# Optimization experiments

Hardware: AMD Instinct MI355X
Metric: run time of the kernel (lower is better)

Reference implementation:

```python
import jax, jax.numpy as jnp
import numpy as np

EMBED = 768
HEADS = 12
HEAD_DIM = EMBED // HEADS  # 64
SCALE = float(EMBED) ** 0.5  # NOTE: module scales by sqrt(embed_size), not sqrt(head_dim)


def setup_inputs() -> dict:
    key = jax.random.key(0)
    k_x, k_wqkv, k_bqkv, k_wp, k_bp = jax.random.split(key, 5)
    x = jax.random.normal(k_x, (16, 1024, EMBED), dtype=jnp.float32)
    # nn.Linear(embed, 3*embed): weight [out,in], bias [out]
    w_qkv = jax.random.normal(k_wqkv, (3 * EMBED, EMBED), dtype=jnp.float32) * 0.02
    b_qkv = jax.random.normal(k_bqkv, (3 * EMBED,), dtype=jnp.float32) * 0.02
    w_proj = jax.random.normal(k_wp, (EMBED, EMBED), dtype=jnp.float32) * 0.02
    b_proj = jax.random.normal(k_bp, (EMBED,), dtype=jnp.float32) * 0.02
    return {"x": x, "w_qkv": w_qkv, "b_qkv": b_qkv, "w_proj": w_proj, "b_proj": b_proj}


def reference(x, w_qkv, b_qkv, w_proj, b_proj):
    B, N, C = x.shape
    qkv = x @ w_qkv.T + b_qkv                       # [B, N, 3C]
    # rearrange 'b n (h d qkv) -> qkv b h n d': qkv index is INNERMOST factor
    qkv = qkv.reshape(B, N, HEADS, HEAD_DIM, 3)
    q = jnp.transpose(qkv[..., 0], (0, 2, 1, 3))    # [B, H, N, D]
    k = jnp.transpose(qkv[..., 1], (0, 2, 1, 3))
    v = jnp.transpose(qkv[..., 2], (0, 2, 1, 3))
    attn = jnp.einsum('bhqd,bhkd->bhqk', q, k) / SCALE
    attn = jax.nn.softmax(attn, axis=-1)
    out = jnp.einsum('bhqk,bhkd->bhqd', attn, v)    # [B, H, N, D]
    out = jnp.transpose(out, (0, 2, 1, 3)).reshape(B, N, C)
    return out @ w_proj.T + b_proj
```

## Files before the change

### kernel.cpp

```cpp
#include <hip/hip_runtime.h>

typedef short bf16x8 __attribute__((ext_vector_type(8)));
typedef float f32x4 __attribute__((ext_vector_type(4)));
typedef float f32x16 __attribute__((ext_vector_type(16)));

#define Q_PRESCALE 0.05205877485199535f

__device__ __forceinline__ unsigned short f2bf(float f) {
  unsigned u = __float_as_uint(f);
  u += 0x7fffu + ((u >> 16) & 1u);
  return (unsigned short)(u >> 16);
}

__device__ __forceinline__ int cvt_pk_bf16(float lo, float hi) {
  int r;
  asm("v_cvt_pk_bf16_f32 %0, %1, %2" : "=v"(r) : "v"(lo), "v"(hi));
  return r;
}

__device__ __forceinline__ float fast_exp2(float x) {
  return __builtin_amdgcn_exp2f(x);
}

__device__ __forceinline__ float cross_half_add(float x) {
  float y;
  asm("v_mov_b32 %0, %1" : "=v"(y) : "v"(x));
  asm("v_permlane32_swap_b32 %0, %1" : "+v"(x), "+v"(y));
  return x + y;
}

__device__ __forceinline__ void gload_lds16(const void* g, void* l) {
  __builtin_amdgcn_global_load_lds(
      (const __attribute__((address_space(1))) void*)g,
      (__attribute__((address_space(3))) void*)l, 16, 0, 0);
}

__global__ __launch_bounds__(256) void prep_kernel(
    const float* __restrict__ x, unsigned short* __restrict__ xb,
    const float* __restrict__ w_qkv, unsigned short* __restrict__ wqkvb,
    const float* __restrict__ w_proj, unsigned short* __restrict__ wprojb) {
  const int bid = blockIdx.x;
  if (bid < 12288) {
    int i = bid * 256 + threadIdx.x;
    float4 v = ((const float4*)x)[i];
    int2 o;
    o.x = cvt_pk_bf16(v.x, v.y);
    o.y = cvt_pk_bf16(v.z, v.w);
    *(int2*)((ushort4*)xb + i) = o;
  } else if (bid < 14016) {
    int i = (bid - 12288) * 256 + threadIdx.x;
    int col = i / 192, i4 = i % 192;
    int c = col / 768, rem = col % 768;
    int h = rem >> 6, d = rem & 63;
    int orig = h * 192 + d * 3 + c;
    float4 v = ((const float4*)(w_qkv + (size_t)orig * 768))[i4];
    int2 o;
    o.x = cvt_pk_bf16(v.x, v.y);
    o.y = cvt_pk_bf16(v.z, v.w);
    *(int2*)((ushort4*)(wqkvb + (size_t)col * 768) + i4) = o;
  } else {
    int i = (bid - 14016) * 256 + threadIdx.x;
    float4 v = ((const float4*)w_proj)[i];
    int2 o;
    o.x = cvt_pk_bf16(v.x, v.y);
    o.y = cvt_pk_bf16(v.z, v.w);
    *(int2*)((ushort4*)wprojb + i) = o;
  }
}

template<int EPI, int NT, int NBUF>
__global__ __launch_bounds__(256) void gemm_bt(
    const unsigned short* __restrict__ A,
    const unsigned short* __restrict__ B,
    const float* __restrict__ bias,
    void* __restrict__ out0,
    unsigned short* __restrict__ Kb,
    unsigned short* __restrict__ VTb) {
  constexpr int K = 768;
  __shared__ __align__(16) unsigned short smem[NBUF * 8192];

  const int tid = threadIdx.x;
  const int w = tid >> 6, lane = tid & 63;
  const int g = lane >> 4, qq = lane & 15;
  const int wr = w >> 1, wc = w & 1;

  const int nwg = gridDim.x, chunk = nwg >> 3;
  const int id = blockIdx.x;
  const int id2 = (id & 7) * chunk + (id >> 3);
  const int bx = id2 % NT, by = id2 / NT;
  const int rowb = by * 128;

  const unsigned short* Ab = A + (size_t)rowb * K;
  const unsigned short* Bb = B + (size_t)bx * 128 * K;

  f32x4 acc[4][4];
#pragma unroll
  for (int i = 0; i < 4; i++)
#pragma unroll
    for (int j = 0; j < 4; j++) acc[i][j] = (f32x4){0.f, 0.f, 0.f, 0.f};

  const int j0 = tid, j1 = tid + 256;
  const int l0 = j0 >> 3, s0 = (j0 & 7) ^ (l0 & 7);
  const int l1 = j1 >> 3, s1 = (j1 & 7) ^ (l1 & 7);
  const size_t off0 = (size_t)(2 * l0 + (s0 >> 2)) * K + (s0 & 3) * 8;
  const size_t off1 = (size_t)(2 * l1 + (s1 >> 2)) * K + (s1 & 3) * 8;

  int aoff[4], boff[4];
#pragma unroll
  for (int mi = 0; mi < 4; mi++) {
    int row = wr * 64 + mi * 16 + qq;
    aoff[mi] = (row >> 1) * 128 + (((g + (row & 1) * 4) ^ ((row >> 1) & 7)) * 16);
    row = wc * 64 + mi * 16 + qq;
    boff[mi] = (row >> 1) * 128 + (((g + (row & 1) * 4) ^ ((row >> 1) & 7)) * 16);
  }

  auto stageg = [&](int sb, int k0) {
    unsigned short* base = &smem[sb * 8192];
    gload_lds16(Ab + off0 + k0, base + j0 * 8);
    gload_lds16(Ab + off1 + k0, base + j1 * 8);
    gload_lds16(Bb + off0 + k0, base + 4096 + j0 * 8);
    gload_lds16(Bb + off1 + k0, base + 4096 + j1 * 8);
  };

#pragma unroll
  for (int p = 0; p < NBUF - 1; ++p) stageg(p, p * 32);

  for (int tg = 0; tg < 24; tg += NBUF) {
#pragma unroll
    for (int j = 0; j < NBUF; ++j) {
      const int t = tg + j;
      if constexpr (NBUF == 3) {
        if (t < 23) asm volatile("s_waitcnt vmcnt(4)" ::: "memory");
        else        asm volatile("s_waitcnt vmcnt(0)" ::: "memory");
      } else {
        if (t < 22)       asm volatile("s_waitcnt vmcnt(8)" ::: "memory");
        else if (t == 22) asm volatile("s_waitcnt vmcnt(4)" ::: "memory");
        else              asm volatile("s_waitcnt vmcnt(0)" ::: "memory");
      }
      asm volatile("s_barrier" ::: "memory");
      if (t <= 24 - NBUF) stageg((j + NBUF - 1) % NBUF, (t + NBUF - 1) * 32);

      const char* Ap = (const char*)&smem[j * 8192];
      const char* Bp = Ap + 8192;
      bf16x8 af[4], bfr[4];
#pragma unroll
      for (int mi = 0; mi < 4; mi++) af[mi] = *(const bf16x8*)(Ap + aoff[mi]);
#pragma unroll
      for (int ni = 0; ni < 4; ni++) bfr[ni] = *(const bf16x8*)(Bp + boff[ni]);
      __builtin_amdgcn_s_setprio(1);
#pragma unroll
      for (int mi = 0; mi < 4; mi++)
#pragma unroll
        for (int ni = 0; ni < 4; ni++)
          acc[mi][ni] = __builtin_amdgcn_mfma_f32_16x16x32_bf16(af[mi], bfr[ni], acc[mi][ni], 0, 0, 0);
      __builtin_amdgcn_s_setprio(0);
    }
  }

  if (EPI == 0) {
    const int c = bx / 6;
    const int h0 = (bx % 6) * 2;
    const int b = rowb >> 10, n0 = rowb & 1023;
    if (c < 2) {
      unsigned short* dst = (c == 0) ? (unsigned short*)out0 : Kb;
      const float scale = (c == 0) ? Q_PRESCALE : 1.0f;
      const int h = h0 + wc;
      const size_t bh = (size_t)(b * 12 + h);
#pragma unroll
      for (int ni = 0; ni < 4; ni++) {
        const int d = ni * 16 + qq;
        const float bv = bias[h * 192 + d * 3 + c];
#pragma unroll
        for (int mi = 0; mi < 4; mi++) {
          const int nb = n0 + wr * 64 + mi * 16 + g * 4;
          unsigned short* base = dst + (bh * 1024 + nb) * 64 + d;
          const int p0 = cvt_pk_bf16((acc[mi][ni][0] + bv) * scale,
                                     (acc[mi][ni][1] + bv) * scale);
          const int p1 = cvt_pk_bf16((acc[mi][ni][2] + bv) * scale,
                                     (acc[mi][ni][3] + bv) * scale);
          base[0]   = (unsigned short)p0;
          base[64]  = (unsigned short)((unsigned)p0 >> 16);
          base[128] = (unsigned short)p1;
          base[192] = (unsigned short)((unsigned)p1 >> 16);
        }
      }
    } else {
      unsigned short* vt = smem;
#pragma unroll
      for (int p = 0; p < 2; ++p) {
        __syncthreads();
        if (wc == p) {
#pragma unroll
          for (int ni = 0; ni < 4; ni++) {
            const int d = ni * 16 + qq;
            const float bv = bias[(h0 + p) * 192 + d * 3 + 2];
#pragma unroll
            for (int mi = 0; mi < 4; mi++) {
              int2 pk;
              pk.x = cvt_pk_bf16(acc[mi][ni][0] + bv, acc[mi][ni][1] + bv);
              pk.y = cvt_pk_bf16(acc[mi][ni][2] + bv, acc[mi][ni][3] + bv);
              *(int2*)&vt[d * 136 + wr * 64 + mi * 16 + g * 4] = pk;
            }
          }
        }
        __syncthreads();
        const size_t bhp = (size_t)(b * 12 + h0 + p);
        const int dd = tid >> 2;
#pragma unroll
        for (int j = 0; j < 4; ++j) {
          const int ch = (tid & 3) + j * 4;
          uint4 vv = *(const uint4*)&vt[dd * 136 + ch * 8];
          const int n = n0 + ch * 8;
          const int tile = n >> 6;
          const int ksd = (n >> 4) & 3;
          const int tk = n & 15;
          *(uint4*)&VTb[bhp * 65536 + (size_t)tile * 4096 + ksd * 1024 + dd * 16 + tk] = vv;
        }
      }
    }
  } else {
    float* O = (float*)out0;
    const int colb = bx * 128 + wc * 64;
#pragma unroll
    for (int ni = 0; ni < 4; ni++) {
      const int col = colb + ni * 16 + qq;
      const float bv = bias[col];
#pragma unroll
      for (int mi = 0; mi < 4; mi++)
#pragma unroll
        for (int r = 0; r < 4; r++) {
          const int row = rowb + wr * 64 + mi * 16 + g * 4 + r;
          O[(size_t)row * 768 + col] = acc[mi][ni][r] + bv;
        }
    }
  }
}

__global__ __launch_bounds__(256, 3) void attn_kernel(
    const unsigned short* __restrict__ Qb,
    const unsigned short* __restrict__ Kb,
    const unsigned short* __restrict__ VTb,
    unsigned short* __restrict__ AO) {
  __shared__ unsigned short Klds[4][4096];
  const int tid = threadIdx.x;
  const int w = tid >> 6, lane = tid & 63;
  const int ql = lane & 31, hi = lane >> 5;

  const int bid = blockIdx.x;
  const int xcd = bid & 7, jj = bid >> 3;
  const int bh = xcd * 24 + (jj >> 3);
  const int qb = jj & 7;
  const int b = bh / 12, h = bh % 12;
  const int q0w = qb * 128 + w * 32;

  const unsigned short* Qh = Qb + (size_t)bh * 65536;
  const unsigned short* Kh = Kb + (size_t)bh * 65536;
  const unsigned short* Vh = VTb + (size_t)bh * 65536;

  bf16x8 qf[4];
#pragma unroll
  for (int ks = 0; ks < 4; ++ks)
    qf[ks] = *(const bf16x8*)&Qh[(size_t)(q0w + ql) * 64 + ks * 16 + hi * 8];

  float l_run = 0.f;
  f32x16 o[2];
#pragma unroll
  for (int dt = 0; dt < 2; ++dt)
#pragma unroll
    for (int i = 0; i < 16; ++i) o[dt][i] = 0.f;

  const int j0 = w * 64 + lane;
  const int r0 = j0 >> 3, s0 = j0 & 7;
  const int g0 = s0 ^ (r0 & 7) ^ ((r0 >> 2) & 6);
  const int sx = (ql & 7) ^ ((ql >> 2) & 6);

  int koff[2][4];
#pragma unroll
  for (int tt = 0; tt < 2; ++tt)
#pragma unroll
    for (int ks = 0; ks < 4; ++ks)
      koff[tt][ks] = (tt * 32 + ql) * 128 + (((ks * 2 + hi) ^ sx) * 16);
  int voff[2][4];
#pragma unroll
  for (int dt = 0; dt < 2; ++dt)
#pragma unroll
    for (int ks = 0; ks < 4; ++ks)
      voff[dt][ks] = ks * 1024 + (dt * 32 + ql) * 16 + hi * 8;

  auto stage = [&](int sb, int t0) {
    gload_lds16(Kh + (size_t)(t0 + r0) * 64 + g0 * 8, &Klds[sb][j0 * 8]);
    gload_lds16(Kh + (size_t)(t0 + r0 + 32) * 64 + g0 * 8, &Klds[sb][j0 * 8 + 2048]);
  };

  stage(0, 0);
  stage(1, 64);
  stage(2, 128);

  for (int t = 0; t < 16; ++t) {
    if (t < 14)      asm volatile("s_waitcnt vmcnt(4)" ::: "memory");
    else if (t == 14) asm volatile("s_waitcnt vmcnt(2)" ::: "memory");
    else              asm volatile("s_waitcnt vmcnt(0)" ::: "memory");
    asm volatile("s_barrier" ::: "memory");
    if (t < 13) stage((t + 3) & 3, (t + 3) * 64);

    const char* Kbuf = (const char*)&Klds[t & 3][0];
    const unsigned short* Vt = Vh + t * 4096;

    bf16x8 vf[2][4];
#pragma unroll
    for (int dt = 0; dt < 2; ++dt)
#pragma unroll
      for (int ks = 0; ks < 4; ++ks)
        vf[dt][ks] = *(const bf16x8*)&Vt[voff[dt][ks]];

    f32x16 s[2];
    __builtin_amdgcn_s_setprio(1);
#pragma unroll
    for (int tt = 0; tt < 2; ++tt) {
#pragma unroll
      for (int i = 0; i < 16; ++i) s[tt][i] = 0.f;
#pragma unroll
      for (int ks = 0; ks < 4; ++ks) {
        bf16x8 ka = *(const bf16x8*)(Kbuf + koff[tt][ks]);
        s[tt] = __builtin_amdgcn_mfma_f32_32x32x16_bf16(ka, qf[ks], s[tt], 0, 0, 0);
      }
    }
    __builtin_amdgcn_s_setprio(0);

#pragma unroll
    for (int tt = 0; tt < 2; ++tt)
#pragma unroll
      for (int i = 0; i < 16; ++i) s[tt][i] = fast_exp2(s[tt][i]);

    float r16[16];
#pragma unroll
    for (int i = 0; i < 16; ++i) r16[i] = s[0][i] + s[1][i];
    float r8[8];
#pragma unroll
    for (int i = 0; i < 8; ++i) r8[i] = r16[i] + r16[i + 8];
    float r4[4];
#pragma unroll
    for (int i = 0; i < 4; ++i) r4[i] = r8[i] + r8[i + 4];
    float rs = (r4[0] + r4[1]) + (r4[2] + r4[3]);
    l_run += cross_half_add(rs);

    union PU { int i[4]; bf16x8 h; };
    PU pb[4];
#pragma unroll
    for (int g16 = 0; g16 < 4; ++g16) {
      const int tt = g16 >> 1, rb = (g16 & 1) * 8;
      int A0, A1, B0, B1;
      float a0 = s[tt][rb + 0], a1 = s[tt][rb + 1], a2 = s[tt][rb + 2], a3 = s[tt][rb + 3];
      float b0 = s[tt][rb + 4], b1 = s[tt][rb + 5], b2 = s[tt][rb + 6], b3 = s[tt][rb + 7];
      asm("v_cvt_pk_bf16_f32 %0, %1, %2" : "=v"(A0) : "v"(a0), "v"(a1));
      asm("v_cvt_pk_bf16_f32 %0, %1, %2" : "=v"(A1) : "v"(a2), "v"(a3));
      asm("v_cvt_pk_bf16_f32 %0, %1, %2" : "=v"(B0) : "v"(b0), "v"(b1));
      asm("v_cvt_pk_bf16_f32 %0, %1, %2" : "=v"(B1) : "v"(b2), "v"(b3));
      asm("v_permlane32_swap_b32 %0, %1" : "+v"(A0), "+v"(B0));
      asm("v_permlane32_swap_b32 %0, %1" : "+v"(A1), "+v"(B1));
      pb[g16].i[0] = A0; pb[g16].i[1] = A1; pb[g16].i[2] = B0; pb[g16].i[3] = B1;
    }

    __builtin_amdgcn_s_setprio(1);
#pragma unroll
    for (int dt = 0; dt < 2; ++dt)
#pragma unroll
      for (int ks = 0; ks < 4; ++ks)
        o[dt] = __builtin_amdgcn_mfma_f32_32x32x16_bf16(vf[dt][ks], pb[ks].h, o[dt], 0, 0, 0);
    __builtin_amdgcn_s_setprio(0);
  }

  const float inv_l = 1.0f / l_run;
  unsigned short* aorow = AO + (size_t)(b * 1024 + q0w + ql) * 768 + h * 64 + hi * 4;
#pragma unroll
  for (int dt = 0; dt < 2; ++dt)
#pragma unroll
    for (int p = 0; p < 4; ++p) {
      int2 vv;
      vv.x = cvt_pk_bf16(o[dt][4 * p + 0] * inv_l, o[dt][4 * p + 1] * inv_l);
      vv.y = cvt_pk_bf16(o[dt][4 * p + 2] * inv_l, o[dt][4 * p + 3] * inv_l);
      *(int2*)&aorow[dt * 32 + 8 * p] = vv;
    }
}

extern "C" void kernel_launch(void* const* d_in, const int* in_sizes, int n_in,
                              void* d_out, int out_size, void* d_ws, size_t ws_size,
                              hipStream_t stream) {
  const float* x      = (const float*)d_in[0];
  const float* w_qkv  = (const float*)d_in[1];
  const float* b_qkv  = (const float*)d_in[2];
  const float* w_proj = (const float*)d_in[3];
  const float* b_proj = (const float*)d_in[4];

  char* ws = (char*)d_ws;
  unsigned short* xb     = (unsigned short*)(ws);
  unsigned short* Qb     = (unsigned short*)(ws + 25165824);
  unsigned short* Kb     = (unsigned short*)(ws + 50331648);
  unsigned short* VTb    = (unsigned short*)(ws + 75497472);
  unsigned short* wqkvb  = (unsigned short*)(ws + 100663296);
  unsigned short* wprojb = (unsigned short*)(ws + 104202240);
  unsigned short* AO = xb;

  prep_kernel<<<14592, 256, 0, stream>>>(x, xb, w_qkv, wqkvb, w_proj, wprojb);

  gemm_bt<0, 18, 4><<<2304, 256, 0, stream>>>(xb, wqkvb, b_qkv, (void*)Qb, Kb, VTb);
  attn_kernel<<<1536, 256, 0, stream>>>(Qb, Kb, VTb, AO);
  gemm_bt<1, 6, 4><<<768, 256, 0, stream>>>(AO, wprojb, b_proj, d_out, nullptr, nullptr);
}
```

Before: 188.3 us.

## Switch K staging to double-buffered 128-key tiles with one barrier per tile

Restructures the attention kernel's K pipeline from a 4-deep ring of 64-key tiles to a 2-deep ring of 128-key tiles. Each iteration now waits for all loads, issues the next tile's prefetch, and processes two 64-key halves, so it runs 8 barriers instead of 16. LDS use stays the same, but prefetch depth drops to one tile and the full vmcnt(0) wait may expose load latency. The V register loads inside each half could also lose overlap with the K prefetch.

```diff
diff --git a/kernel.cpp b/kernel.cpp
--- a/kernel.cpp
+++ b/kernel.cpp
@@ -241,7 +241,7 @@
     const unsigned short* __restrict__ Kb,
     const unsigned short* __restrict__ VTb,
     unsigned short* __restrict__ AO) {
-  __shared__ unsigned short Klds[4][4096];
+  __shared__ unsigned short Klds[2][8192];
   const int tid = threadIdx.x;
   const int w = tid >> 6, lane = tid & 63;
   const int ql = lane & 31, hi = lane >> 5;
@@ -269,9 +269,14 @@
 #pragma unroll
     for (int i = 0; i < 16; ++i) o[dt][i] = 0.f;
 
-  const int j0 = w * 64 + lane;
-  const int r0 = j0 >> 3, s0 = j0 & 7;
-  const int g0 = s0 ^ (r0 & 7) ^ ((r0 >> 2) & 6);
+  int kgofs[4];
+#pragma unroll
+  for (int k = 0; k < 4; ++k) {
+    const int j = tid + k * 256;
+    const int r = j >> 3, s = j & 7;
+    const int g0 = s ^ (r & 7) ^ ((r >> 2) & 6);
+    kgofs[k] = r * 64 + g0 * 8;
+  }
   const int sx = (ql & 7) ^ ((ql >> 2) & 6);
 
   int koff[2][4];
@@ -287,87 +292,90 @@
     for (int ks = 0; ks < 4; ++ks)
       voff[dt][ks] = ks * 1024 + (dt * 32 + ql) * 16 + hi * 8;
 
-  auto stage = [&](int sb, int t0) {
-    gload_lds16(Kh + (size_t)(t0 + r0) * 64 + g0 * 8, &Klds[sb][j0 * 8]);
-    gload_lds16(Kh + (size_t)(t0 + r0 + 32) * 64 + g0 * 8, &Klds[sb][j0 * 8 + 2048]);
+  auto stage = [&](int sb, int t) {
+    const unsigned short* Kt = Kh + (size_t)t * 8192;
+#pragma unroll
+    for (int k = 0; k < 4; ++k)
+      gload_lds16(Kt + kgofs[k], &Klds[sb][(tid + k * 256) * 8]);
   };
 
   stage(0, 0);
-  stage(1, 64);
-  stage(2, 128);
-
-  for (int t = 0; t < 16; ++t) {
-    if (t < 14)      asm volatile("s_waitcnt vmcnt(4)" ::: "memory");
-    else if (t == 14) asm volatile("s_waitcnt vmcnt(2)" ::: "memory");
-    else              asm volatile("s_waitcnt vmcnt(0)" ::: "memory");
+
+  for (int t = 0; t < 8; ++t) {
+    asm volatile("s_waitcnt vmcnt(0)" ::: "memory");
     asm volatile("s_barrier" ::: "memory");
-    if (t < 13) stage((t + 3) & 3, (t + 3) * 64);
-
-    const char* Kbuf = (const char*)&Klds[t & 3][0];
-    const unsigned short* Vt = Vh + t * 4096;
-
-    bf16x8 vf[2][4];
-#pragma unroll
-    for (int dt = 0; dt < 2; ++dt)
-#pragma unroll
-      for (int ks = 0; ks < 4; ++ks)
-        vf[dt][ks] = *(const bf16x8*)&Vt[voff[dt][ks]];
-
-    f32x16 s[2];
-    __builtin_amdgcn_s_setprio(1);
-#pragma unroll
-    for (int tt = 0; tt < 2; ++tt) {
-#pragma unroll
-      for (int i = 0; i < 16; ++i) s[tt][i] = 0.f;
-#pragma unroll
-      for (int ks = 0; ks < 4; ++ks) {
-        bf16x8 ka = *(const bf16x8*)(Kbuf + koff[tt][ks]);
-        s[tt] = __builtin_amdgcn_mfma_f32_32x32x16_bf16(ka, qf[ks], s[tt], 0, 0, 0);
+    if (t < 7) stage((t + 1) & 1, t + 1);
+
+    const char* Kbuf = (const char*)&Klds[t & 1][0];
+
+#pragma unroll
+    for (int half = 0; half < 2; ++half) {
+      const int kb = half * 8192;
+      const unsigned short* Vt = Vh + (size_t)t * 8192 + half * 4096;
+
+      bf16x8 vf[2][4];
+#pragma unroll
+      for (int dt = 0; dt < 2; ++dt)
+#pragma unroll
+        for (int ks = 0; ks < 4; ++ks)
+          vf[dt][ks] = *(const bf16x8*)&Vt[voff[dt][ks]];
+
+      f32x16 s[2];
+      __builtin_amdgcn_s_setprio(1);
+#pragma unroll
+      for (int tt = 0; tt < 2; ++tt) {
+#pragma unroll
+        for (int i = 0; i < 16; ++i) s[tt][i] = 0.f;
+#pragma unroll
+        for (int ks = 0; ks < 4; ++ks) {
+          bf16x8 ka = *(const bf16x8*)(Kbuf + kb + koff[tt][ks]);
+          s[tt] = __builtin_amdgcn_mfma_f32_32x32x16_bf16(ka, qf[ks], s[tt], 0, 0, 0);
+        }
       }
+      __builtin_amdgcn_s_setprio(0);
+
+#pragma unroll
+      for (int tt = 0; tt < 2; ++tt)
+#pragma unroll
+        for (int i = 0; i < 16; ++i) s[tt][i] = fast_exp2(s[tt][i]);
+
+      float r16[16];
+#pragma unroll
+      for (int i = 0; i < 16; ++i) r16[i] = s[0][i] + s[1][i];
+      float r8[8];
+#pragma unroll
+      for (int i = 0; i < 8; ++i) r8[i] = r16[i] + r16[i + 8];
+      float r4[4];
+#pragma unroll
+      for (int i = 0; i < 4; ++i) r4[i] = r8[i] + r8[i + 4];
+      float rs = (r4[0] + r4[1]) + (r4[2] + r4[3]);
+      l_run += cross_half_add(rs);
+
+      union PU { int i[4]; bf16x8 h; };
+      PU pb[4];
+#pragma unroll
+      for (int g16 = 0; g16 < 4; ++g16) {
+        const int tt = g16 >> 1, rb = (g16 & 1) * 8;
+        int A0, A1, B0, B1;
+        float a0 = s[tt][rb + 0], a1 = s[tt][rb + 1], a2 = s[tt][rb + 2], a3 = s[tt][rb + 3];
+        float b0 = s[tt][rb + 4], b1 = s[tt][rb + 5], b2 = s[tt][rb + 6], b3 = s[tt][rb + 7];
+        asm("v_cvt_pk_bf16_f32 %0, %1, %2" : "=v"(A0) : "v"(a0), "v"(a1));
+        asm("v_cvt_pk_bf16_f32 %0, %1, %2" : "=v"(A1) : "v"(a2), "v"(a3));
+        asm("v_cvt_pk_bf16_f32 %0, %1, %2" : "=v"(B0) : "v"(b0), "v"(b1));
+        asm("v_cvt_pk_bf16_f32 %0, %1, %2" : "=v"(B1) : "v"(b2), "v"(b3));
+        asm("v_permlane32_swap_b32 %0, %1" : "+v"(A0), "+v"(B0));
+        asm("v_permlane32_swap_b32 %0, %1" : "+v"(A1), "+v"(B1));
+        pb[g16].i[0] = A0; pb[g16].i[1] = A1; pb[g16].i[2] = B0; pb[g16].i[3] = B1;
+      }
+
+      __builtin_amdgcn_s_setprio(1);
+#pragma unroll
+      for (int dt = 0; dt < 2; ++dt)
+#pragma unroll
+        for (int ks = 0; ks < 4; ++ks)
+          o[dt] = __builtin_amdgcn_mfma_f32_32x32x16_bf16(vf[dt][ks], pb[ks].h, o[dt], 0, 0, 0);
+      __builtin_amdgcn_s_setprio(0);
     }
-    __builtin_amdgcn_s_setprio(0);
-
-#pragma unroll
-    for (int tt = 0; tt < 2; ++tt)
-#pragma unroll
-      for (int i = 0; i < 16; ++i) s[tt][i] = fast_exp2(s[tt][i]);
-
-    float r16[16];
-#pragma unroll
-    for (int i = 0; i < 16; ++i) r16[i] = s[0][i] + s[1][i];
-    float r8[8];
-#pragma unroll
-    for (int i = 0; i < 8; ++i) r8[i] = r16[i] + r16[i + 8];
-    float r4[4];
-#pragma unroll
-    for (int i = 0; i < 4; ++i) r4[i] = r8[i] + r8[i + 4];
-    float rs = (r4[0] + r4[1]) + (r4[2] + r4[3]);
-    l_run += cross_half_add(rs);
-
-    union PU { int i[4]; bf16x8 h; };
-    PU pb[4];
-#pragma unroll
-    for (int g16 = 0; g16 < 4; ++g16) {
-      const int tt = g16 >> 1, rb = (g16 & 1) * 8;
-      int A0, A1, B0, B1;
-      float a0 = s[tt][rb + 0], a1 = s[tt][rb + 1], a2 = s[tt][rb + 2], a3 = s[tt][rb + 3];
-      float b0 = s[tt][rb + 4], b1 = s[tt][rb + 5], b2 = s[tt][rb + 6], b3 = s[tt][rb + 7];
-      asm("v_cvt_pk_bf16_f32 %0, %1, %2" : "=v"(A0) : "v"(a0), "v"(a1));
-      asm("v_cvt_pk_bf16_f32 %0, %1, %2" : "=v"(A1) : "v"(a2), "v"(a3));
-      asm("v_cvt_pk_bf16_f32 %0, %1, %2" : "=v"(B0) : "v"(b0), "v"(b1));
-      asm("v_cvt_pk_bf16_f32 %0, %1, %2" : "=v"(B1) : "v"(b2), "v"(b3));
-      asm("v_permlane32_swap_b32 %0, %1" : "+v"(A0), "+v"(B0));
-      asm("v_permlane32_swap_b32 %0, %1" : "+v"(A1), "+v"(B1));
-      pb[g16].i[0] = A0; pb[g16].i[1] = A1; pb[g16].i[2] = B0; pb[g16].i[3] = B1;
-    }
-
-    __builtin_amdgcn_s_setprio(1);
-#pragma unroll
-    for (int dt = 0; dt < 2; ++dt)
-#pragma unroll
-      for (int ks = 0; ks < 4; ++ks)
-        o[dt] = __builtin_amdgcn_mfma_f32_32x32x16_bf16(vf[dt][ks], pb[ks].h, o[dt], 0, 0, 0);
-    __builtin_amdgcn_s_setprio(0);
   }
 
   const float inv_l = 1.0f / l_run;
```

New measurement: 193.8 us. +2.9%, slower.
